# Performance work log

Hardware: AMD Instinct MI355X
Metric: run time of the kernel (lower is better)

The kernel has to match this reference:

```python
import jax, jax.numpy as jnp
import numpy as np
import math

B, N, D = 2, 2048, 1024
H = 16
HD = D // H
WINDOW = 256
LN_EPS = 1e-5
NEG_INF = float('-inf')


def _alibi_slopes(num_heads):
    # num_heads=16 is a power of two -> no extra-slope branch
    closest = 2 ** math.floor(math.log2(num_heads))
    base = 2.0 ** (-(2.0 ** (-(math.log2(closest) - 3))))
    return np.power(base, np.arange(1, closest + 1, dtype=np.float32))


def setup_inputs() -> dict:
    key = jax.random.key(0)
    ks = jax.random.split(key, 8)
    s = 0.02
    return {
        'x': jax.random.normal(ks[0], (B, N, D), dtype=jnp.float32),
        'qkv_w': jax.random.normal(ks[1], (D, 3 * D), dtype=jnp.float32) * s,
        'qkv_b': jnp.zeros((3 * D,), jnp.float32),
        'proj_w': jax.random.normal(ks[2], (D, D), dtype=jnp.float32) * s,
        'proj_b': jnp.zeros((D,), jnp.float32),
        'ln1_g': jnp.ones((D,), jnp.float32),
        'ln1_b': jnp.zeros((D,), jnp.float32),
        'ln2_g': jnp.ones((D,), jnp.float32),
        'ln2_b': jnp.zeros((D,), jnp.float32),
        'fc1_w': jax.random.normal(ks[3], (D, 4 * D), dtype=jnp.float32) * s,
        'fc1_b': jnp.zeros((4 * D,), jnp.float32),
        'fc2_w': jax.random.normal(ks[4], (4 * D, D), dtype=jnp.float32) * s,
        'fc2_b': jnp.zeros((D,), jnp.float32),
    }


def _layernorm(x, g, b):
    mu = jnp.mean(x, axis=-1, keepdims=True)
    var = jnp.mean(jnp.square(x - mu), axis=-1, keepdims=True)
    return (x - mu) * jax.lax.rsqrt(var + LN_EPS) * g + b


def reference(x, qkv_w, qkv_b, proj_w, proj_b, ln1_g, ln1_b, ln2_g, ln2_b,
              fc1_w, fc1_b, fc2_w, fc2_b):
    # ---- ALiBi sliding-window causal attention (pre-norm) ----
    h = _layernorm(x, ln1_g, ln1_b)
    qkv = (h @ qkv_w + qkv_b).reshape(B, N, 3, H, HD)
    q, k, v = [jnp.transpose(qkv[:, :, i], (0, 2, 1, 3)) for i in range(3)]  # [B,H,N,HD]

    scale = HD ** -0.5
    attn = jnp.einsum('bhqd,bhkd->bhqk', q, k) * scale  # [B,H,N,N]

    pos = jnp.arange(N)
    rel = pos[None, :] - pos[:, None]                      # rel[i,j] = j - i
    slopes = jnp.asarray(_alibi_slopes(H))                 # [H]
    a = slopes[:, None, None] * jnp.abs(rel).astype(jnp.float32)
    alibi = jnp.where(rel < 0, -a, a)                      # == slopes * rel
    attn = attn + alibi[None]

    # sliding-window mask: +1.0 inside window (faithful to ones-init), -inf outside
    sw = jnp.where(jnp.abs(rel) >= WINDOW, NEG_INF, 1.0)
    attn = attn + sw[None, None]

    # causal mask
    attn = jnp.where((rel > 0)[None, None], NEG_INF, attn)

    p = jax.nn.softmax(attn, axis=-1)
    o = jnp.einsum('bhqk,bhkd->bhqd', p, v)
    o = jnp.transpose(o, (0, 2, 1, 3)).reshape(B, N, D)
    x = x + (o @ proj_w + proj_b)

    # ---- FFN (Linear -> exact GELU -> Linear), pre-norm residual ----
    h2 = _layernorm(x, ln2_g, ln2_b)
    ff = jax.nn.gelu(h2 @ fc1_w + fc1_b, approximate=False) @ fc2_w + fc2_b
    return x + ff
```

## Files before the change

kernel.cpp:

```cpp
#include <hip/hip_runtime.h>
#include <stdint.h>

typedef unsigned short u16;
typedef __attribute__((ext_vector_type(8))) short bf16x8;
typedef __attribute__((ext_vector_type(4))) float f32x4;

__device__ __forceinline__ u16 f2bf(float f) {
  union { float f; unsigned u; } x; x.f = f;
  unsigned r = x.u + 0x7fffu + ((x.u >> 16) & 1u);
  return (u16)(r >> 16);
}

#define GLOAD16(g, l) __builtin_amdgcn_global_load_lds( \
    (const __attribute__((address_space(1))) unsigned int*)(g), \
    (__attribute__((address_space(3))) unsigned int*)(l), 16, 0, 0)

__global__ __launch_bounds__(256) void wt_kernel(const float* __restrict__ W,
                                                 u16* __restrict__ Wt, int K, int N) {
  __shared__ float tile[32][33];
  int tx = threadIdx.x & 31, ty = threadIdx.x >> 5;
  int n0 = blockIdx.x * 32, k0 = blockIdx.y * 32;
#pragma unroll
  for (int i = 0; i < 32; i += 8)
    tile[ty + i][tx] = W[(size_t)(k0 + ty + i) * N + n0 + tx];
  __syncthreads();
#pragma unroll
  for (int i = 0; i < 32; i += 8)
    Wt[(size_t)(n0 + ty + i) * K + k0 + tx] = f2bf(tile[tx][ty + i]);
}

__global__ __launch_bounds__(256) void ln_kernel(const float* __restrict__ x,
                                                 const float* __restrict__ g,
                                                 const float* __restrict__ be,
                                                 u16* __restrict__ out) {
  int row = blockIdx.x, t = threadIdx.x;
  const float4 v = ((const float4*)(x + (size_t)row * 1024))[t];
  float s = v.x + v.y + v.z + v.w;
#pragma unroll
  for (int m = 1; m < 64; m <<= 1) s += __shfl_xor(s, m);
  __shared__ float p1[4], p2[4];
  int wid = t >> 6, lane = t & 63;
  if (lane == 0) p1[wid] = s;
  __syncthreads();
  float mean = (p1[0] + p1[1] + p1[2] + p1[3]) * (1.f / 1024.f);
  float a0 = v.x - mean, a1 = v.y - mean, a2 = v.z - mean, a3 = v.w - mean;
  float ss = a0 * a0 + a1 * a1 + a2 * a2 + a3 * a3;
#pragma unroll
  for (int m = 1; m < 64; m <<= 1) ss += __shfl_xor(ss, m);
  if (lane == 0) p2[wid] = ss;
  __syncthreads();
  float var = (p2[0] + p2[1] + p2[2] + p2[3]) * (1.f / 1024.f);
  float rs = rsqrtf(var + 1e-5f);
  const float4 gg = ((const float4*)g)[t];
  const float4 bb = ((const float4*)be)[t];
  ushort4 ov;
  ov.x = f2bf(a0 * rs * gg.x + bb.x);
  ov.y = f2bf(a1 * rs * gg.y + bb.y);
  ov.z = f2bf(a2 * rs * gg.z + bb.z);
  ov.w = f2bf(a3 * rs * gg.w + bb.w);
  *(ushort4*)(out + (size_t)row * 1024 + t * 4) = ov;
}

template <int GELU_F, int HAS_RES, int OUT_F32, int OUT_BF16>
__global__ __launch_bounds__(256) void gemm_kernel(
    const u16* __restrict__ A, const u16* __restrict__ Bt,
    const float* __restrict__ bias, const float* __restrict__ res,
    float* __restrict__ outf, u16* __restrict__ outb, int M, int N, int K) {
  __shared__ u16 lA[128 * 64];
  __shared__ u16 lB[128 * 64];
  const int t = threadIdx.x, lane = t & 63, wid = t >> 6;
  const int bm = blockIdx.x, bn = blockIdx.y;
  const int wr = wid >> 1, wc = wid & 1;
  f32x4 acc[4][4] = {};

  const int nkt = K >> 6;
  for (int kt = 0; kt < nkt; ++kt) {
#pragma unroll
    for (int r = 0; r < 4; ++r) {
      int f = (r * 256 + t) * 16;
      int fs = f ^ (((f >> 7) & 7) << 4);
      int row = fs >> 7;
      int kb = (fs & 127) >> 1;
      const u16* gA = A + (size_t)(bm * 128 + row) * K + kt * 64 + kb;
      const u16* gB = Bt + (size_t)(bn * 128 + row) * K + kt * 64 + kb;
      GLOAD16(gA, ((char*)lA) + (r * 256 + wid * 64) * 16);
      GLOAD16(gB, ((char*)lB) + (r * 256 + wid * 64) * 16);
    }
    __syncthreads();
#pragma unroll
    for (int kk = 0; kk < 2; ++kk) {
      bf16x8 af[4], bfr[4];
#pragma unroll
      for (int fm = 0; fm < 4; ++fm) {
        int row = wr * 64 + fm * 16 + (lane & 15);
        int k = kk * 32 + (lane >> 4) * 8;
        af[fm] = *(const bf16x8*)((const char*)lA + ((row * 128 + k * 2) ^ ((row & 7) << 4)));
      }
#pragma unroll
      for (int fn = 0; fn < 4; ++fn) {
        int row = wc * 64 + fn * 16 + (lane & 15);
        int k = kk * 32 + (lane >> 4) * 8;
        bfr[fn] = *(const bf16x8*)((const char*)lB + ((row * 128 + k * 2) ^ ((row & 7) << 4)));
      }
#pragma unroll
      for (int fm = 0; fm < 4; ++fm)
#pragma unroll
        for (int fn = 0; fn < 4; ++fn)
          acc[fm][fn] = __builtin_amdgcn_mfma_f32_16x16x32_bf16(af[fm], bfr[fn], acc[fm][fn], 0, 0, 0);
    }
    __syncthreads();
  }

#pragma unroll
  for (int fm = 0; fm < 4; ++fm) {
#pragma unroll
    for (int fn = 0; fn < 4; ++fn) {
      int col = bn * 128 + wc * 64 + fn * 16 + (lane & 15);
      float bcol = bias[col];
#pragma unroll
      for (int r = 0; r < 4; ++r) {
        int row = bm * 128 + wr * 64 + fm * 16 + (lane >> 4) * 4 + r;
        float v = acc[fm][fn][r] + bcol;
        if constexpr (GELU_F) v = 0.5f * v * (1.0f + erff(v * 0.70710678118654752f));
        size_t idx = (size_t)row * N + col;
        if constexpr (HAS_RES) v += res[idx];
        if constexpr (OUT_F32) outf[idx] = v;
        if constexpr (OUT_BF16) outb[idx] = f2bf(v);
      }
    }
  }
}

__global__ __launch_bounds__(256) void attn_kernel(const u16* __restrict__ qkv,
                                                   u16* __restrict__ o) {
  __shared__ u16 lK[320 * 64];
  __shared__ u16 lV[64 * 344];
  __shared__ u16 lP[4][16 * 296];
  const int t = threadIdx.x, lane = t & 63, w = t >> 6;
  const int qtile = blockIdx.x, bh = blockIdx.y, b = bh >> 4, h = bh & 15;
  const int kbase = qtile * 64 - 256;
  const size_t bq = (size_t)b * 2048 * 3072;
  const float NEGBIG = -1e30f;

  for (int r = 0; r < 11; ++r) {
    int jl = r * 32 + (t >> 3);
    int d0 = (t & 7) * 8;
    int jg = kbase + jl;
    if (jl < 336) {
      uint4 vv;
      if (jg >= 0 && jg < 2048)
        vv = *(const uint4*)(qkv + bq + (size_t)jg * 3072 + 2048 + h * 64 + d0);
      else
        vv = make_uint4(0, 0, 0, 0);
      const u16* vs = (const u16*)&vv;
#pragma unroll
      for (int u = 0; u < 8; ++u) lV[(d0 + u) * 344 + jl] = vs[u];
      if (jl < 320) {
        uint4 kv;
        if (jg >= 0 && jg < 2048)
          kv = *(const uint4*)(qkv + bq + (size_t)jg * 3072 + 1024 + h * 64 + d0);
        else
          kv = make_uint4(0, 0, 0, 0);
        *(uint4*)((char*)lK + ((jl * 128 + d0 * 2) ^ ((jl & 7) << 4))) = kv;
      }
    }
  }
  __syncthreads();

  const int i0 = qtile * 64 + w * 16;
  const int q15 = lane & 15, grp = lane >> 4;
  const u16* qrow = qkv + bq + (size_t)(i0 + q15) * 3072 + h * 64;
  bf16x8 qf0 = *(const bf16x8*)(qrow + grp * 8);
  bf16x8 qf1 = *(const bf16x8*)(qrow + 32 + grp * 8);

  f32x4 st[17];
#pragma unroll
  for (int tt = 0; tt < 17; ++tt) {
    st[tt] = f32x4{0.f, 0.f, 0.f, 0.f};
    int klb = w * 16 + tt * 16;
#pragma unroll
    for (int kk = 0; kk < 2; ++kk) {
      int row = klb + q15;
      int k = kk * 32 + grp * 8;
      bf16x8 kf = *(const bf16x8*)((const char*)lK + ((row * 128 + k * 2) ^ ((row & 7) << 4)));
      st[tt] = __builtin_amdgcn_mfma_f32_16x16x32_bf16(kf, (kk ? qf1 : qf0), st[tt], 0, 0, 0);
    }
  }

  const float slope = exp2f(-0.5f * (float)(h + 1));
  const int qg = i0 + q15;
  float mx = NEGBIG;
#pragma unroll
  for (int tt = 0; tt < 17; ++tt) {
    int kb = kbase + w * 16 + tt * 16;
#pragma unroll
    for (int r = 0; r < 4; ++r) {
      int key = kb + grp * 4 + r;
      float s = st[tt][r] * 0.125f + slope * (float)(key - qg);
      bool valid = (key >= 0) && (key <= qg) && (qg - key < 256);
      s = valid ? s : NEGBIG;
      st[tt][r] = s;
      mx = fmaxf(mx, s);
    }
  }
  mx = fmaxf(mx, __shfl_xor(mx, 16));
  mx = fmaxf(mx, __shfl_xor(mx, 32));
  float sum = 0.f;
#pragma unroll
  for (int tt = 0; tt < 17; ++tt)
#pragma unroll
    for (int r = 0; r < 4; ++r) {
      float p = __expf(st[tt][r] - mx);
      st[tt][r] = p;
      sum += p;
    }
  sum += __shfl_xor(sum, 16);
  sum += __shfl_xor(sum, 32);
  const float inv = 1.0f / sum;

  u16* Pw = &lP[w][0];
#pragma unroll
  for (int tt = 0; tt < 17; ++tt) {
    unsigned u0 = ((unsigned)f2bf(st[tt][1]) << 16) | f2bf(st[tt][0]);
    unsigned u1 = ((unsigned)f2bf(st[tt][3]) << 16) | f2bf(st[tt][2]);
    uint2 uu; uu.x = u0; uu.y = u1;
    *(uint2*)(Pw + q15 * 296 + tt * 16 + grp * 4) = uu;
  }
  { uint2 z; z.x = 0; z.y = 0; *(uint2*)(Pw + q15 * 296 + 272 + grp * 4) = z; }

  f32x4 ot[4] = {};
#pragma unroll
  for (int c = 0; c < 9; ++c) {
    bf16x8 pf = *(const bf16x8*)(Pw + q15 * 296 + c * 32 + grp * 8);
#pragma unroll
    for (int hb = 0; hb < 4; ++hb) {
      bf16x8 vf = *(const bf16x8*)(lV + (hb * 16 + q15) * 344 + w * 16 + c * 32 + grp * 8);
      ot[hb] = __builtin_amdgcn_mfma_f32_16x16x32_bf16(vf, pf, ot[hb], 0, 0, 0);
    }
  }

#pragma unroll
  for (int hb = 0; hb < 4; ++hb) {
    ushort4 ov;
    ov.x = f2bf(ot[hb][0] * inv);
    ov.y = f2bf(ot[hb][1] * inv);
    ov.z = f2bf(ot[hb][2] * inv);
    ov.w = f2bf(ot[hb][3] * inv);
    *(ushort4*)(o + (size_t)(b * 2048 + i0 + q15) * 1024 + h * 64 + hb * 16 + grp * 4) = ov;
  }
}

extern "C" void kernel_launch(void* const* d_in, const int* in_sizes, int n_in,
                              void* d_out, int out_size, void* d_ws, size_t ws_size,
                              hipStream_t stream) {
  const float* x      = (const float*)d_in[0];
  const float* qkv_w  = (const float*)d_in[1];
  const float* qkv_b  = (const float*)d_in[2];
  const float* proj_w = (const float*)d_in[3];
  const float* proj_b = (const float*)d_in[4];
  const float* ln1_g  = (const float*)d_in[5];
  const float* ln1_b  = (const float*)d_in[6];
  const float* ln2_g  = (const float*)d_in[7];
  const float* ln2_b  = (const float*)d_in[8];
  const float* fc1_w  = (const float*)d_in[9];
  const float* fc1_b  = (const float*)d_in[10];
  const float* fc2_w  = (const float*)d_in[11];
  const float* fc2_b  = (const float*)d_in[12];
  float* out = (float*)d_out;

  char* ws = (char*)d_ws;
  u16* qkvw_t  = (u16*)(ws);
  u16* projw_t = (u16*)(ws + 6291456);
  u16* fc1w_t  = (u16*)(ws + 8388608);
  u16* fc2w_t  = (u16*)(ws + 16777216);
  char* BIG    = ws + 25165824;
  char* SMALL  = ws + 58720256;
  u16* qkvb = (u16*)BIG;
  u16* ff1  = (u16*)BIG;
  u16* h1   = (u16*)SMALL;
  u16* obuf = (u16*)SMALL;
  u16* h2   = (u16*)SMALL;
  float* x1 = out;

  wt_kernel<<<dim3(96, 32), 256, 0, stream>>>(qkv_w, qkvw_t, 1024, 3072);
  wt_kernel<<<dim3(32, 32), 256, 0, stream>>>(proj_w, projw_t, 1024, 1024);
  wt_kernel<<<dim3(128, 32), 256, 0, stream>>>(fc1_w, fc1w_t, 1024, 4096);
  wt_kernel<<<dim3(32, 128), 256, 0, stream>>>(fc2_w, fc2w_t, 4096, 1024);

  ln_kernel<<<4096, 256, 0, stream>>>(x, ln1_g, ln1_b, h1);
  gemm_kernel<0, 0, 0, 1><<<dim3(32, 24), 256, 0, stream>>>(h1, qkvw_t, qkv_b, nullptr, nullptr, qkvb, 4096, 3072, 1024);
  attn_kernel<<<dim3(32, 32), 256, 0, stream>>>(qkvb, obuf);
  gemm_kernel<0, 1, 1, 0><<<dim3(32, 8), 256, 0, stream>>>(obuf, projw_t, proj_b, x, x1, nullptr, 4096, 1024, 1024);
  ln_kernel<<<4096, 256, 0, stream>>>(x1, ln2_g, ln2_b, h2);
  gemm_kernel<1, 0, 0, 1><<<dim3(32, 32), 256, 0, stream>>>(h2, fc1w_t, fc1_b, nullptr, nullptr, ff1, 4096, 4096, 1024);
  gemm_kernel<0, 1, 1, 0><<<dim3(32, 8), 256, 0, stream>>>(ff1, fc2w_t, fc2_b, x1, out, nullptr, 4096, 1024, 4096);
}
```

Baseline: 387.6 us.

## Double-buffer GEMM LDS tiles, narrow N tiles for D-output GEMMs, alias attention K/V LDS

The GEMM kernel now keeps two LDS buffers. It issues the global-to-LDS loads for the next K tile before computing on the current one, so memory latency overlaps the MFMA work. A BN template parameter adds a 128x64 tile variant, used for the proj and fc2 GEMMs with N=1024, which doubles their block count to 512 and fills more CUs. The attention kernel now loads K first, computes scores and softmax, then reuses the same LDS region for V, which lowers LDS usage per block. The cost is that the V load now runs after the softmax instead of overlapping it, and the double-buffered GEMM uses twice the LDS, which may lower occupancy.

```diff
diff --git a/kernel.cpp b/kernel.cpp
--- a/kernel.cpp
+++ b/kernel.cpp
@@ -61,49 +61,66 @@
   *(ushort4*)(out + (size_t)row * 1024 + t * 4) = ov;
 }
 
-template <int GELU_F, int HAS_RES, int OUT_F32, int OUT_BF16>
+template <int BN, int GELU_F, int HAS_RES, int OUT_F32, int OUT_BF16>
 __global__ __launch_bounds__(256) void gemm_kernel(
     const u16* __restrict__ A, const u16* __restrict__ Bt,
     const float* __restrict__ bias, const float* __restrict__ res,
     float* __restrict__ outf, u16* __restrict__ outb, int M, int N, int K) {
-  __shared__ u16 lA[128 * 64];
-  __shared__ u16 lB[128 * 64];
+  __shared__ u16 lA[2][128 * 64];
+  __shared__ u16 lB[2][BN * 64];
   const int t = threadIdx.x, lane = t & 63, wid = t >> 6;
   const int bm = blockIdx.x, bn = blockIdx.y;
-  const int wr = wid >> 1, wc = wid & 1;
-  f32x4 acc[4][4] = {};
+  constexpr int FM = (BN == 128) ? 4 : 2;
+  const int wr = (BN == 128) ? (wid >> 1) : wid;
+  const int wc = (BN == 128) ? (wid & 1) : 0;
+  f32x4 acc[FM][4] = {};
 
   const int nkt = K >> 6;
-  for (int kt = 0; kt < nkt; ++kt) {
+
+  auto stage = [&](int buf, int kt) {
 #pragma unroll
     for (int r = 0; r < 4; ++r) {
       int f = (r * 256 + t) * 16;
       int fs = f ^ (((f >> 7) & 7) << 4);
       int row = fs >> 7;
       int kb = (fs & 127) >> 1;
-      const u16* gA = A + (size_t)(bm * 128 + row) * K + kt * 64 + kb;
-      const u16* gB = Bt + (size_t)(bn * 128 + row) * K + kt * 64 + kb;
-      GLOAD16(gA, ((char*)lA) + (r * 256 + wid * 64) * 16);
-      GLOAD16(gB, ((char*)lB) + (r * 256 + wid * 64) * 16);
-    }
-    __syncthreads();
+      GLOAD16(A + (size_t)(bm * 128 + row) * K + kt * 64 + kb,
+              ((char*)&lA[buf][0]) + (r * 256 + wid * 64) * 16);
+    }
+#pragma unroll
+    for (int r = 0; r < BN / 32; ++r) {
+      int f = (r * 256 + t) * 16;
+      int fs = f ^ (((f >> 7) & 7) << 4);
+      int row = fs >> 7;
+      int kb = (fs & 127) >> 1;
+      GLOAD16(Bt + (size_t)(bn * BN + row) * K + kt * 64 + kb,
+              ((char*)&lB[buf][0]) + (r * 256 + wid * 64) * 16);
+    }
+  };
+
+  stage(0, 0);
+  __syncthreads();
+
+  for (int kt = 0; kt < nkt; ++kt) {
+    const int cur = kt & 1;
+    if (kt + 1 < nkt) stage(cur ^ 1, kt + 1);
 #pragma unroll
     for (int kk = 0; kk < 2; ++kk) {
-      bf16x8 af[4], bfr[4];
-#pragma unroll
-      for (int fm = 0; fm < 4; ++fm) {
-        int row = wr * 64 + fm * 16 + (lane & 15);
+      bf16x8 af[FM], bfr[4];
+#pragma unroll
+      for (int fm = 0; fm < FM; ++fm) {
+        int row = wr * (FM * 16) + fm * 16 + (lane & 15);
         int k = kk * 32 + (lane >> 4) * 8;
-        af[fm] = *(const bf16x8*)((const char*)lA + ((row * 128 + k * 2) ^ ((row & 7) << 4)));
+        af[fm] = *(const bf16x8*)((const char*)&lA[cur][0] + ((row * 128 + k * 2) ^ ((row & 7) << 4)));
       }
 #pragma unroll
       for (int fn = 0; fn < 4; ++fn) {
         int row = wc * 64 + fn * 16 + (lane & 15);
         int k = kk * 32 + (lane >> 4) * 8;
-        bfr[fn] = *(const bf16x8*)((const char*)lB + ((row * 128 + k * 2) ^ ((row & 7) << 4)));
+        bfr[fn] = *(const bf16x8*)((const char*)&lB[cur][0] + ((row * 128 + k * 2) ^ ((row & 7) << 4)));
       }
 #pragma unroll
-      for (int fm = 0; fm < 4; ++fm)
+      for (int fm = 0; fm < FM; ++fm)
 #pragma unroll
         for (int fn = 0; fn < 4; ++fn)
           acc[fm][fn] = __builtin_amdgcn_mfma_f32_16x16x32_bf16(af[fm], bfr[fn], acc[fm][fn], 0, 0, 0);
@@ -112,14 +129,14 @@
   }
 
 #pragma unroll
-  for (int fm = 0; fm < 4; ++fm) {
+  for (int fm = 0; fm < FM; ++fm) {
 #pragma unroll
     for (int fn = 0; fn < 4; ++fn) {
-      int col = bn * 128 + wc * 64 + fn * 16 + (lane & 15);
+      int col = bn * BN + wc * 64 + fn * 16 + (lane & 15);
       float bcol = bias[col];
 #pragma unroll
       for (int r = 0; r < 4; ++r) {
-        int row = bm * 128 + wr * 64 + fm * 16 + (lane >> 4) * 4 + r;
+        int row = bm * 128 + wr * (FM * 16) + fm * 16 + (lane >> 4) * 4 + r;
         float v = acc[fm][fn][r] + bcol;
         if constexpr (GELU_F) v = 0.5f * v * (1.0f + erff(v * 0.70710678118654752f));
         size_t idx = (size_t)row * N + col;
@@ -133,14 +150,91 @@
 
 __global__ __launch_bounds__(256) void attn_kernel(const u16* __restrict__ qkv,
                                                    u16* __restrict__ o) {
-  __shared__ u16 lK[320 * 64];
-  __shared__ u16 lV[64 * 344];
+  __shared__ u16 kvbuf[22016];
   __shared__ u16 lP[4][16 * 296];
+  u16* lK = kvbuf;
+  u16* lV = kvbuf;
   const int t = threadIdx.x, lane = t & 63, w = t >> 6;
   const int qtile = blockIdx.x, bh = blockIdx.y, b = bh >> 4, h = bh & 15;
   const int kbase = qtile * 64 - 256;
   const size_t bq = (size_t)b * 2048 * 3072;
   const float NEGBIG = -1e30f;
+
+  for (int r = 0; r < 10; ++r) {
+    int jl = r * 32 + (t >> 3);
+    int d0 = (t & 7) * 8;
+    int jg = kbase + jl;
+    uint4 kv;
+    if (jg >= 0 && jg < 2048)
+      kv = *(const uint4*)(qkv + bq + (size_t)jg * 3072 + 1024 + h * 64 + d0);
+    else
+      kv = make_uint4(0, 0, 0, 0);
+    *(uint4*)((char*)lK + ((jl * 128 + d0 * 2) ^ ((jl & 7) << 4))) = kv;
+  }
+  __syncthreads();
+
+  const int i0 = qtile * 64 + w * 16;
+  const int q15 = lane & 15, grp = lane >> 4;
+  const u16* qrow = qkv + bq + (size_t)(i0 + q15) * 3072 + h * 64;
+  bf16x8 qf0 = *(const bf16x8*)(qrow + grp * 8);
+  bf16x8 qf1 = *(const bf16x8*)(qrow + 32 + grp * 8);
+
+  f32x4 st[17];
+#pragma unroll
+  for (int tt = 0; tt < 17; ++tt) {
+    st[tt] = f32x4{0.f, 0.f, 0.f, 0.f};
+    int klb = w * 16 + tt * 16;
+#pragma unroll
+    for (int kk = 0; kk < 2; ++kk) {
+      int row = klb + q15;
+      int k = kk * 32 + grp * 8;
+      bf16x8 kf = *(const bf16x8*)((const char*)lK + ((row * 128 + k * 2) ^ ((row & 7) << 4)));
+      st[tt] = __builtin_amdgcn_mfma_f32_16x16x32_bf16(kf, (kk ? qf1 : qf0), st[tt], 0, 0, 0);
+    }
+  }
+
+  const float slope = exp2f(-0.5f * (float)(h + 1));
+  const int qg = i0 + q15;
+  float mx = NEGBIG;
+#pragma unroll
+  for (int tt = 0; tt < 17; ++tt) {
+    int kb = kbase + w * 16 + tt * 16;
+#pragma unroll
+    for (int r = 0; r < 4; ++r) {
+      int key = kb + grp * 4 + r;
+      float s = st[tt][r] * 0.125f + slope * (float)(key - qg);
+      bool valid = (key >= 0) && (key <= qg) && (qg - key < 256);
+      s = valid ? s : NEGBIG;
+      st[tt][r] = s;
+      mx = fmaxf(mx, s);
+    }
+  }
+  mx = fmaxf(mx, __shfl_xor(mx, 16));
+  mx = fmaxf(mx, __shfl_xor(mx, 32));
+  float sum = 0.f;
+#pragma unroll
+  for (int tt = 0; tt < 17; ++tt)
+#pragma unroll
+    for (int r = 0; r < 4; ++r) {
+      float p = __expf(st[tt][r] - mx);
+      st[tt][r] = p;
+      sum += p;
+    }
+  sum += __shfl_xor(sum, 16);
+  sum += __shfl_xor(sum, 32);
+  const float inv = 1.0f / sum;
+
+  u16* Pw = &lP[w][0];
+#pragma unroll
+  for (int tt = 0; tt < 17; ++tt) {
+    unsigned u0 = ((unsigned)f2bf(st[tt][1]) << 16) | f2bf(st[tt][0]);
+    unsigned u1 = ((unsigned)f2bf(st[tt][3]) << 16) | f2bf(st[tt][2]);
+    uint2 uu; uu.x = u0; uu.y = u1;
+    *(uint2*)(Pw + q15 * 296 + tt * 16 + grp * 4) = uu;
+  }
+  { uint2 z; z.x = 0; z.y = 0; *(uint2*)(Pw + q15 * 296 + 272 + grp * 4) = z; }
+
+  __syncthreads();
 
   for (int r = 0; r < 11; ++r) {
     int jl = r * 32 + (t >> 3);
@@ -155,78 +249,9 @@
       const u16* vs = (const u16*)&vv;
 #pragma unroll
       for (int u = 0; u < 8; ++u) lV[(d0 + u) * 344 + jl] = vs[u];
-      if (jl < 320) {
-        uint4 kv;
-        if (jg >= 0 && jg < 2048)
-          kv = *(const uint4*)(qkv + bq + (size_t)jg * 3072 + 1024 + h * 64 + d0);
-        else
-          kv = make_uint4(0, 0, 0, 0);
-        *(uint4*)((char*)lK + ((jl * 128 + d0 * 2) ^ ((jl & 7) << 4))) = kv;
-      }
-    }
-  }
-  __syncthreads();
-
-  const int i0 = qtile * 64 + w * 16;
-  const int q15 = lane & 15, grp = lane >> 4;
-  const u16* qrow = qkv + bq + (size_t)(i0 + q15) * 3072 + h * 64;
-  bf16x8 qf0 = *(const bf16x8*)(qrow + grp * 8);
-  bf16x8 qf1 = *(const bf16x8*)(qrow + 32 + grp * 8);
-
-  f32x4 st[17];
-#pragma unroll
-  for (int tt = 0; tt < 17; ++tt) {
-    st[tt] = f32x4{0.f, 0.f, 0.f, 0.f};
-    int klb = w * 16 + tt * 16;
-#pragma unroll
-    for (int kk = 0; kk < 2; ++kk) {
-      int row = klb + q15;
-      int k = kk * 32 + grp * 8;
-      bf16x8 kf = *(const bf16x8*)((const char*)lK + ((row * 128 + k * 2) ^ ((row & 7) << 4)));
-      st[tt] = __builtin_amdgcn_mfma_f32_16x16x32_bf16(kf, (kk ? qf1 : qf0), st[tt], 0, 0, 0);
-    }
-  }
-
-  const float slope = exp2f(-0.5f * (float)(h + 1));
-  const int qg = i0 + q15;
-  float mx = NEGBIG;
-#pragma unroll
-  for (int tt = 0; tt < 17; ++tt) {
-    int kb = kbase + w * 16 + tt * 16;
-#pragma unroll
-    for (int r = 0; r < 4; ++r) {
-      int key = kb + grp * 4 + r;
-      float s = st[tt][r] * 0.125f + slope * (float)(key - qg);
-      bool valid = (key >= 0) && (key <= qg) && (qg - key < 256);
-      s = valid ? s : NEGBIG;
-      st[tt][r] = s;
-      mx = fmaxf(mx, s);
-    }
-  }
-  mx = fmaxf(mx, __shfl_xor(mx, 16));
-  mx = fmaxf(mx, __shfl_xor(mx, 32));
-  float sum = 0.f;
-#pragma unroll
-  for (int tt = 0; tt < 17; ++tt)
-#pragma unroll
-    for (int r = 0; r < 4; ++r) {
-      float p = __expf(st[tt][r] - mx);
-      st[tt][r] = p;
-      sum += p;
-    }
-  sum += __shfl_xor(sum, 16);
-  sum += __shfl_xor(sum, 32);
-  const float inv = 1.0f / sum;
-
-  u16* Pw = &lP[w][0];
-#pragma unroll
-  for (int tt = 0; tt < 17; ++tt) {
-    unsigned u0 = ((unsigned)f2bf(st[tt][1]) << 16) | f2bf(st[tt][0]);
-    unsigned u1 = ((unsigned)f2bf(st[tt][3]) << 16) | f2bf(st[tt][2]);
-    uint2 uu; uu.x = u0; uu.y = u1;
-    *(uint2*)(Pw + q15 * 296 + tt * 16 + grp * 4) = uu;
-  }
-  { uint2 z; z.x = 0; z.y = 0; *(uint2*)(Pw + q15 * 296 + 272 + grp * 4) = z; }
+    }
+  }
+  __syncthreads();
 
   f32x4 ot[4] = {};
 #pragma unroll
@@ -288,10 +313,10 @@
   wt_kernel<<<dim3(32, 128), 256, 0, stream>>>(fc2_w, fc2w_t, 4096, 1024);
 
   ln_kernel<<<4096, 256, 0, stream>>>(x, ln1_g, ln1_b, h1);
-  gemm_kernel<0, 0, 0, 1><<<dim3(32, 24), 256, 0, stream>>>(h1, qkvw_t, qkv_b, nullptr, nullptr, qkvb, 4096, 3072, 1024);
+  gemm_kernel<128, 0, 0, 0, 1><<<dim3(32, 24), 256, 0, stream>>>(h1, qkvw_t, qkv_b, nullptr, nullptr, qkvb, 4096, 3072, 1024);
   attn_kernel<<<dim3(32, 32), 256, 0, stream>>>(qkvb, obuf);
-  gemm_kernel<0, 1, 1, 0><<<dim3(32, 8), 256, 0, stream>>>(obuf, projw_t, proj_b, x, x1, nullptr, 4096, 1024, 1024);
+  gemm_kernel<64, 0, 1, 1, 0><<<dim3(32, 16), 256, 0, stream>>>(obuf, projw_t, proj_b, x, x1, nullptr, 4096, 1024, 1024);
   ln_kernel<<<4096, 256, 0, stream>>>(x1, ln2_g, ln2_b, h2);
-  gemm_kernel<1, 0, 0, 1><<<dim3(32, 32), 256, 0, stream>>>(h2, fc1w_t, fc1_b, nullptr, nullptr, ff1, 4096, 4096, 1024);
-  gemm_kernel<0, 1, 1, 0><<<dim3(32, 8), 256, 0, stream>>>(ff1, fc2w_t, fc2_b, x1, out, nullptr, 4096, 1024, 4096);
-}
+  gemm_kernel<128, 1, 0, 0, 1><<<dim3(32, 32), 256, 0, stream>>>(h2, fc1w_t, fc1_b, nullptr, nullptr, ff1, 4096, 4096, 1024);
+  gemm_kernel<64, 0, 1, 1, 0><<<dim3(32, 16), 256, 0, stream>>>(ff1, fc2w_t, fc2_b, x1, out, nullptr, 4096, 1024, 4096);
+}
```

Measured after the change: 332.1 us. -14.3%, faster.
